# Kernel tuning notes

Measured on AMD Instinct MI355X. Metric: run time of the kernel, lower is better.

## Reference

```python
import jax, jax.numpy as jnp
import numpy as np

D_IN = 768
D_OUT = 768
NUM_HEADS = 12


def setup_inputs() -> dict:
    key = jax.random.key(0)
    kx, kq, kk, kv, ko = jax.random.split(key, 5)
    x = jax.random.normal(kx, (4, 2048, D_IN), dtype=jnp.float32)
    # torch.rand -> uniform [0,1)
    w_query = jax.random.uniform(kq, (D_IN, D_OUT), dtype=jnp.float32)
    w_key = jax.random.uniform(kk, (D_IN, D_OUT), dtype=jnp.float32)
    w_value = jax.random.uniform(kv, (D_IN, D_OUT), dtype=jnp.float32)
    out_proj = jax.random.uniform(ko, (D_IN, D_OUT), dtype=jnp.float32)
    return {"x": x, "w_query": w_query, "w_key": w_key, "w_value": w_value, "out_proj": out_proj}


def reference(x, w_query, w_key, w_value, out_proj):
    b, n, _ = x.shape
    hd = D_OUT // NUM_HEADS  # head_dim
    q = (x @ w_query).reshape(b, n, NUM_HEADS, hd).transpose(0, 2, 1, 3)  # [b,h,n,hd]
    k = (x @ w_key).reshape(b, n, NUM_HEADS, hd).transpose(0, 2, 1, 3)
    v = (x @ w_value).reshape(b, n, NUM_HEADS, hd).transpose(0, 2, 1, 3)
    scores = jnp.einsum('bhqd,bhkd->bhqk', q, k)
    causal = jnp.triu(jnp.ones((n, n), dtype=bool), k=1)
    scores = jnp.where(causal, -jnp.inf, scores)
    attn = jax.nn.softmax(scores / jnp.sqrt(jnp.float32(hd)), axis=-1)
    # dropout p=0.0 -> identity
    ctx = jnp.einsum('bhqk,bhkd->bhqd', attn, v).transpose(0, 2, 1, 3).reshape(b, n, D_OUT)
    return ctx @ out_proj
```

## Files before the change

### kernel.cpp

```cpp
#include <hip/hip_runtime.h>

typedef __bf16    bf16x8 __attribute__((ext_vector_type(8)));
typedef __bf16    bf16x4 __attribute__((ext_vector_type(4)));
typedef _Float16  f16x8  __attribute__((ext_vector_type(8)));
typedef float     f32x4  __attribute__((ext_vector_type(4)));

#define MFMA16(a,b,c)  __builtin_amdgcn_mfma_f32_16x16x32_bf16((a),(b),(c),0,0,0)
#define MFMAF16(a,b,c) __builtin_amdgcn_mfma_f32_16x16x32_f16((a),(b),(c),0,0,0)

#define AS1(p) (const __attribute__((address_space(1))) void*)(p)
#define AS3(p) (__attribute__((address_space(3))) void*)(p)
#define GLL16(g, l) __builtin_amdgcn_global_load_lds(AS1(g), AS3(l), 16, 0, 0)

__device__ __forceinline__ float fexp2(float x) {
  float r; asm("v_exp_f32 %0, %1" : "=v"(r) : "v"(x)); return r;
}

#define QSCALE 0.18033688011112042f

__global__ __launch_bounds__(256) void k_conv_x(const float* __restrict__ x,
                                                __bf16* __restrict__ xh,
                                                __bf16* __restrict__ xl) {
  int i = blockIdx.x * 256 + threadIdx.x;
  const float4* p = (const float4*)x + (size_t)i * 2;
  float4 a = p[0], b = p[1];
  float v[8] = {a.x, a.y, a.z, a.w, b.x, b.y, b.z, b.w};
  bf16x8 h, l;
#pragma unroll
  for (int j = 0; j < 8; ++j) {
    __bf16 hh = (__bf16)v[j];
    h[j] = hh;
    l[j] = (__bf16)(v[j] - (float)hh);
  }
  *(bf16x8*)(xh + (size_t)i * 8) = h;
  *(bf16x8*)(xl + (size_t)i * 8) = l;
}

__global__ __launch_bounds__(256) void k_conv_w(const float* __restrict__ wq,
                                                const float* __restrict__ wk,
                                                const float* __restrict__ wv,
                                                const float* __restrict__ op,
                                                __bf16* __restrict__ wt_h,
                                                __bf16* __restrict__ wt_l,
                                                __bf16* __restrict__ wot) {
  __shared__ float tile[32][33];
  int bid = blockIdx.x;
  int m = bid / 576, rem = bid % 576;
  int tr = rem / 24, tc = rem % 24;
  const float* src = (m == 0) ? wq : (m == 1) ? wk : (m == 2) ? wv : op;
  int tx = threadIdx.x & 31, ty = threadIdx.x >> 5;
  int r0 = tr * 32, c0 = tc * 32;
#pragma unroll
  for (int j = 0; j < 4; ++j)
    tile[ty + j * 8][tx] = src[(size_t)(r0 + ty + j * 8) * 768 + c0 + tx];
  __syncthreads();
#pragma unroll
  for (int j = 0; j < 4; ++j) {
    float v = tile[tx][ty + j * 8];
    size_t o = (size_t)(c0 + ty + j * 8) * 768 + r0 + tx;
    if (m < 3) {
      size_t oo = (size_t)m * (768 * 768) + o;
      __bf16 h = (__bf16)v;
      wt_h[oo] = h;
      wt_l[oo] = (__bf16)(v - (float)h);
    } else {
      wot[o] = (__bf16)v;
    }
  }
}

__global__ __launch_bounds__(256) void k_qkv_gemm(
    const __bf16* __restrict__ Ah, const __bf16* __restrict__ Al,
    const __bf16* __restrict__ Bh, const __bf16* __restrict__ Bl,
    _Float16* __restrict__ qf_o, _Float16* __restrict__ kf_o,
    __bf16* __restrict__ vT_o) {
  __shared__ __align__(16) __bf16 AsH[2][128 * 32];
  __shared__ __align__(16) __bf16 AsL[2][128 * 32];
  __shared__ __align__(16) __bf16 BsH[2][128 * 32];
  __shared__ __align__(16) __bf16 BsL[2][128 * 32];
  int t = threadIdx.x, lane = t & 63, wid = t >> 6;
  int l15 = lane & 15, lh = lane >> 4;
  int bid = blockIdx.x;
  int mt = bid & 63, nt = bid >> 6;
  int m0 = mt * 128, n0 = nt * 128;
  int wr = wid >> 1, wc = wid & 1;
  bool split = (n0 < 1536);
  f32x4 acc[4][4];
#pragma unroll
  for (int i = 0; i < 4; ++i)
#pragma unroll
    for (int j = 0; j < 4; ++j) acc[i][j] = (f32x4){0.f, 0.f, 0.f, 0.f};

  int row0 = t >> 2;
  int kkA = (((t & 3) ^ ((row0 >> 1) & 3)) << 3);
  char* lAH[2] = {(char*)AsH[0] + wid * 1024, (char*)AsH[1] + wid * 1024};
  char* lAL[2] = {(char*)AsL[0] + wid * 1024, (char*)AsL[1] + wid * 1024};
  char* lBH[2] = {(char*)BsH[0] + wid * 1024, (char*)BsH[1] + wid * 1024};
  char* lBL[2] = {(char*)BsL[0] + wid * 1024, (char*)BsL[1] + wid * 1024};

#define QKV_STAGE(bb, k0s) do {                                              \
    size_t a0 = (size_t)(m0 + row0) * 768 + (k0s) + kkA;                     \
    size_t a1 = a0 + (size_t)64 * 768;                                       \
    size_t b0 = (size_t)(n0 + row0) * 768 + (k0s) + kkA;                     \
    size_t b1 = b0 + (size_t)64 * 768;                                       \
    GLL16(Ah + a0, lAH[bb]); GLL16(Ah + a1, lAH[bb] + 4096);                 \
    GLL16(Bh + b0, lBH[bb]); GLL16(Bh + b1, lBH[bb] + 4096);                 \
    if (split) {                                                             \
      GLL16(Al + a0, lAL[bb]); GLL16(Al + a1, lAL[bb] + 4096);               \
      GLL16(Bl + b0, lBL[bb]); GLL16(Bl + b1, lBL[bb] + 4096);               \
    }                                                                        \
  } while (0)

  QKV_STAGE(0, 0);
  asm volatile("s_waitcnt vmcnt(0)" ::: "memory");
  __syncthreads();

  for (int tt = 0; tt < 24; ++tt) {
    int cur = tt & 1;
    if (tt < 23) QKV_STAGE(cur ^ 1, (tt + 1) * 32);

    bf16x8 af[4], alf[4], bf_[4], blf[4];
#pragma unroll
    for (int i = 0; i < 4; ++i) {
      int rowA = wr * 64 + i * 16 + l15;
      int aoff = rowA * 64 + (((lh ^ (rowA >> 1)) & 3) << 4);
      int rowB = wc * 64 + i * 16 + l15;
      int boff = rowB * 64 + (((lh ^ (rowB >> 1)) & 3) << 4);
      af[i]  = *(const bf16x8*)((char*)AsH[cur] + aoff);
      bf_[i] = *(const bf16x8*)((char*)BsH[cur] + boff);
      if (split) {
        alf[i] = *(const bf16x8*)((char*)AsL[cur] + aoff);
        blf[i] = *(const bf16x8*)((char*)BsL[cur] + boff);
      }
    }
#pragma unroll
    for (int i = 0; i < 4; ++i)
#pragma unroll
      for (int j = 0; j < 4; ++j) {
        acc[i][j] = MFMA16(af[i], bf_[j], acc[i][j]);
        if (split) {
          acc[i][j] = MFMA16(af[i], blf[j], acc[i][j]);
          acc[i][j] = MFMA16(alf[i], bf_[j], acc[i][j]);
        }
      }
    asm volatile("s_waitcnt vmcnt(0)" ::: "memory");
    __syncthreads();
  }
#undef QKV_STAGE

#pragma unroll
  for (int j = 0; j < 4; ++j) {
    int c = n0 + wc * 64 + j * 16 + l15;
    int which = c / 768; int cc = c - which * 768;
    int hh = cc >> 6, d = cc & 63;
#pragma unroll
    for (int i = 0; i < 4; ++i)
#pragma unroll
      for (int r = 0; r < 4; ++r) {
        int m = m0 + wr * 64 + i * 16 + lh * 4 + r;
        int bb = m >> 11, n = m & 2047;
        float v = acc[i][j][r];
        if (which == 2) {
          vT_o[((size_t)(bb * 12 + hh) * 64 + d) * 2048 + n] = (__bf16)v;
        } else {
          size_t o = ((size_t)(bb * 12 + hh) * 2048 + n) * 64 + d;
          if (which == 0) qf_o[o] = (_Float16)(v * QSCALE);
          else            kf_o[o] = (_Float16)v;
        }
      }
  }
}

__global__ __launch_bounds__(256) void k_attn(
    const _Float16* __restrict__ Qf, const _Float16* __restrict__ Kf,
    const __bf16* __restrict__ Vt, __bf16* __restrict__ ctx) {
  __shared__ __align__(16) _Float16 Ks[2][64 * 64];
  __shared__ __align__(16) __bf16 Vs[2][64 * 64];
  __shared__ __align__(16) __bf16 Pt[4][32 * 64];
  int t = threadIdx.x, lane = t & 63, wid = t >> 6;
  int l15 = lane & 15, lh = lane >> 4;
  int bid = blockIdx.x;
  int bh = bid % 48;
  int qt = 15 - bid / 48;
  int qbase = qt * 128 + wid * 32;
  size_t base = (size_t)bh * (2048 * 64);
  char* ptw = (char*)Pt[wid];

  int skey = t >> 3, sdb = t & 7;
  int ssw = (sdb ^ (skey & 7)) * 8;
  const _Float16* ksrc = Kf + base + (size_t)skey * 64 + ssw;
  const __bf16* vsrc = Vt + base + (size_t)skey * 2048 + ssw;
  char* dK[2] = {(char*)Ks[0] + wid * 1024, (char*)Ks[1] + wid * 1024};
  char* dV[2] = {(char*)Vs[0] + wid * 1024, (char*)Vs[1] + wid * 1024};

#define ATT_STAGE(bb, k0s) do {                                    \
    GLL16(ksrc + (size_t)(k0s) * 64, dK[bb]);                      \
    GLL16(ksrc + (size_t)(k0s) * 64 + 2048, dK[bb] + 4096);        \
    GLL16(vsrc + (k0s), dV[bb]);                                   \
    GLL16(vsrc + (k0s) + 32 * 2048, dV[bb] + 4096);                \
  } while (0)

  f16x8 qf[2][2];
#pragma unroll
  for (int i = 0; i < 2; ++i)
#pragma unroll
    for (int kk = 0; kk < 2; ++kk)
      qf[i][kk] = *(const f16x8*)(Qf + base +
          (size_t)(qbase + i * 16 + l15) * 64 + kk * 32 + lh * 8);

  f32x4 o[2][4];
#pragma unroll
  for (int i = 0; i < 2; ++i)
#pragma unroll
    for (int d = 0; d < 4; ++d) o[i][d] = (f32x4){0.f, 0.f, 0.f, 0.f};
  float mrun[2] = {-1e30f, -1e30f}, lrun[2] = {0.f, 0.f};

  int nIter = 2 * qt + 2;
  ATT_STAGE(0, 0);
  asm volatile("s_waitcnt vmcnt(0)" ::: "memory");
  __syncthreads();

  for (int it = 0; it < nIter; ++it) {
    int cur = it & 1;
    int k0 = it * 64;
    if (it + 1 < nIter) ATT_STAGE(cur ^ 1, k0 + 64);

    if (k0 <= qbase + 31) {
      f32x4 s[4][2];
#pragma unroll
      for (int j = 0; j < 4; ++j)
#pragma unroll
        for (int i = 0; i < 2; ++i) s[j][i] = (f32x4){0.f, 0.f, 0.f, 0.f};
#pragma unroll
      for (int j = 0; j < 4; ++j) {
        int kr = j * 16 + l15;
#pragma unroll
        for (int kk = 0; kk < 2; ++kk) {
          int sw = ((kk * 4 + lh) ^ (kr & 7)) << 4;
          f16x8 kf = *(const f16x8*)((char*)Ks[cur] + kr * 128 + sw);
          s[j][0] = MFMAF16(kf, qf[0][kk], s[j][0]);
          s[j][1] = MFMAF16(kf, qf[1][kk], s[j][1]);
        }
      }

      if (k0 + 63 > qbase) {
#pragma unroll
        for (int j = 0; j < 4; ++j)
#pragma unroll
          for (int i = 0; i < 2; ++i)
#pragma unroll
            for (int r = 0; r < 4; ++r) {
              int key = k0 + j * 16 + lh * 4 + r;
              int qg = qbase + i * 16 + l15;
              if (key > qg) s[j][i][r] = -1e30f;
            }
      }

#pragma unroll
      for (int i = 0; i < 2; ++i) {
        float m01 = fmaxf(fmaxf(s[0][i][0], s[0][i][1]), fmaxf(s[0][i][2], s[0][i][3]));
        float m23 = fmaxf(fmaxf(s[1][i][0], s[1][i][1]), fmaxf(s[1][i][2], s[1][i][3]));
        float m45 = fmaxf(fmaxf(s[2][i][0], s[2][i][1]), fmaxf(s[2][i][2], s[2][i][3]));
        float m67 = fmaxf(fmaxf(s[3][i][0], s[3][i][1]), fmaxf(s[3][i][2], s[3][i][3]));
        float mx = fmaxf(fmaxf(m01, m23), fmaxf(m45, m67));
        mx = fmaxf(mx, __shfl_xor(mx, 16));
        mx = fmaxf(mx, __shfl_xor(mx, 32));
        float mn = fmaxf(mrun[i], mx);
        float alpha = fexp2(mrun[i] - mn);
        mrun[i] = mn;
        float rsum = 0.f;
#pragma unroll
        for (int j = 0; j < 4; ++j)
#pragma unroll
          for (int r = 0; r < 4; ++r) {
            float e = fexp2(s[j][i][r] - mn);
            s[j][i][r] = e;
            rsum += e;
          }
        rsum += __shfl_xor(rsum, 16);
        rsum += __shfl_xor(rsum, 32);
        lrun[i] = lrun[i] * alpha + rsum;
#pragma unroll
        for (int d = 0; d < 4; ++d) o[i][d] *= alpha;
#pragma unroll
        for (int j = 0; j < 4; ++j) {
          bf16x4 pk = { (__bf16)s[j][i][0], (__bf16)s[j][i][1],
                        (__bf16)s[j][i][2], (__bf16)s[j][i][3] };
          int row = 16 * i + l15;
          int boff = (row * 128 + j * 32 + lh * 8) ^ ((l15 & 7) << 4);
          *(bf16x4*)(ptw + boff) = pk;
        }
      }
      asm volatile("" ::: "memory");
      bf16x8 pa[2][2];
#pragma unroll
      for (int i = 0; i < 2; ++i)
#pragma unroll
        for (int kk = 0; kk < 2; ++kk) {
          int row = 16 * i + l15;
          int boff = (row * 128 + kk * 64 + lh * 16) ^ ((l15 & 7) << 4);
          pa[i][kk] = *(const bf16x8*)(ptw + boff);
        }
      asm volatile("" ::: "memory");

#pragma unroll
      for (int dt = 0; dt < 4; ++dt) {
        int dr = dt * 16 + l15;
#pragma unroll
        for (int kk = 0; kk < 2; ++kk) {
          int sw = ((kk * 4 + lh) ^ (dr & 7)) << 4;
          bf16x8 vf = *(const bf16x8*)((char*)Vs[cur] + dr * 128 + sw);
          o[0][dt] = MFMA16(vf, pa[0][kk], o[0][dt]);
          o[1][dt] = MFMA16(vf, pa[1][kk], o[1][dt]);
        }
      }
    }
    asm volatile("s_waitcnt vmcnt(0)" ::: "memory");
    __syncthreads();
  }
#undef ATT_STAGE

  int b = bh / 12, hh = bh - (bh / 12) * 12;
  float inv[2] = {1.f / lrun[0], 1.f / lrun[1]};
#pragma unroll
  for (int i = 0; i < 2; ++i)
#pragma unroll
    for (int dt = 0; dt < 4; ++dt) {
      bf16x4 cw = { (__bf16)(o[i][dt][0] * inv[i]), (__bf16)(o[i][dt][1] * inv[i]),
                    (__bf16)(o[i][dt][2] * inv[i]), (__bf16)(o[i][dt][3] * inv[i]) };
      int row = 16 * i + l15;
      int boff = (row * 128 + dt * 32 + lh * 8) ^ ((l15 & 7) << 4);
      *(bf16x4*)(ptw + boff) = cw;
    }
  asm volatile("" ::: "memory");
  int lr = lane >> 1, hc = lane & 1;
#pragma unroll
  for (int q16 = 0; q16 < 4; ++q16) {
    int boff = (lr * 128 + hc * 64 + q16 * 16) ^ ((lr & 7) << 4);
    bf16x8 vv = *(const bf16x8*)(ptw + boff);
    *(bf16x8*)(ctx + ((size_t)b * 2048 + qbase + lr) * 768 + hh * 64 + hc * 32 + q16 * 8) = vv;
  }
}

__global__ __launch_bounds__(256) void k_out_gemm(const __bf16* __restrict__ A,
                                                  const __bf16* __restrict__ Bt,
                                                  float* __restrict__ C) {
  __shared__ __align__(16) __bf16 As[2][128 * 32];
  __shared__ __align__(16) __bf16 Bs[2][128 * 32];
  int t = threadIdx.x, lane = t & 63, wid = t >> 6;
  int l15 = lane & 15, lh = lane >> 4;
  int bid = blockIdx.x;
  int mt = bid & 63, nt = bid >> 6;
  int m0 = mt * 128, n0 = nt * 128;
  int wr = wid >> 1, wc = wid & 1;
  f32x4 acc[4][4];
#pragma unroll
  for (int i = 0; i < 4; ++i)
#pragma unroll
    for (int j = 0; j < 4; ++j) acc[i][j] = (f32x4){0.f, 0.f, 0.f, 0.f};
  int row0 = t >> 2;
  int kkA = (((t & 3) ^ ((row0 >> 1) & 3)) << 3);
  char* lA[2] = {(char*)As[0] + wid * 1024, (char*)As[1] + wid * 1024};
  char* lB[2] = {(char*)Bs[0] + wid * 1024, (char*)Bs[1] + wid * 1024};

#define OUT_STAGE(bb, k0s) do {                                              \
    size_t a0 = (size_t)(m0 + row0) * 768 + (k0s) + kkA;                     \
    size_t b0 = (size_t)(n0 + row0) * 768 + (k0s) + kkA;                     \
    GLL16(A + a0, lA[bb]);  GLL16(A + a0 + (size_t)64 * 768, lA[bb] + 4096); \
    GLL16(Bt + b0, lB[bb]); GLL16(Bt + b0 + (size_t)64 * 768, lB[bb] + 4096);\
  } while (0)

  OUT_STAGE(0, 0);
  asm volatile("s_waitcnt vmcnt(0)" ::: "memory");
  __syncthreads();

  for (int tt = 0; tt < 24; ++tt) {
    int cur = tt & 1;
    if (tt < 23) OUT_STAGE(cur ^ 1, (tt + 1) * 32);
    bf16x8 af[4], bf_[4];
#pragma unroll
    for (int i = 0; i < 4; ++i) {
      int rowA = wr * 64 + i * 16 + l15;
      int aoff = rowA * 64 + (((lh ^ (rowA >> 1)) & 3) << 4);
      int rowB = wc * 64 + i * 16 + l15;
      int boff = rowB * 64 + (((lh ^ (rowB >> 1)) & 3) << 4);
      af[i]  = *(const bf16x8*)((char*)As[cur] + aoff);
      bf_[i] = *(const bf16x8*)((char*)Bs[cur] + boff);
    }
#pragma unroll
    for (int i = 0; i < 4; ++i)
#pragma unroll
      for (int j = 0; j < 4; ++j) acc[i][j] = MFMA16(af[i], bf_[j], acc[i][j]);
    asm volatile("s_waitcnt vmcnt(0)" ::: "memory");
    __syncthreads();
  }
#undef OUT_STAGE

#pragma unroll
  for (int j = 0; j < 4; ++j) {
    int c = n0 + wc * 64 + j * 16 + l15;
#pragma unroll
    for (int i = 0; i < 4; ++i)
#pragma unroll
      for (int r = 0; r < 4; ++r) {
        int m = m0 + wr * 64 + i * 16 + lh * 4 + r;
        C[(size_t)m * 768 + c] = acc[i][j][r];
      }
  }
}

extern "C" void kernel_launch(void* const* d_in, const int* in_sizes, int n_in,
                              void* d_out, int out_size, void* d_ws, size_t ws_size,
                              hipStream_t stream) {
  const float* x  = (const float*)d_in[0];
  const float* wq = (const float*)d_in[1];
  const float* wk = (const float*)d_in[2];
  const float* wv = (const float*)d_in[3];
  const float* op = (const float*)d_in[4];
  float* out = (float*)d_out;

  char* ws = (char*)d_ws;
  const size_t SZ = (size_t)8192 * 768 * 2;
  __bf16* xh     = (__bf16*)ws;    ws += SZ;
  __bf16* xl     = (__bf16*)ws;    ws += SZ;
  __bf16* wt_h   = (__bf16*)ws;    ws += (size_t)2304 * 768 * 2;
  __bf16* wt_l   = (__bf16*)ws;    ws += (size_t)2304 * 768 * 2;
  __bf16* wot    = (__bf16*)ws;    ws += (size_t)768 * 768 * 2;
  _Float16* qf   = (_Float16*)ws;  ws += SZ;
  _Float16* kf   = (_Float16*)ws;  ws += SZ;
  __bf16* vT     = (__bf16*)ws;    ws += SZ;
  __bf16* ctx    = (__bf16*)ws;    ws += SZ;

  hipLaunchKernelGGL(k_conv_x, dim3(3072), dim3(256), 0, stream, x, xh, xl);
  hipLaunchKernelGGL(k_conv_w, dim3(2304), dim3(256), 0, stream,
                     wq, wk, wv, op, wt_h, wt_l, wot);
  hipLaunchKernelGGL(k_qkv_gemm, dim3(64 * 18), dim3(256), 0, stream,
                     xh, xl, wt_h, wt_l, qf, kf, vT);
  hipLaunchKernelGGL(k_attn, dim3(48 * 16), dim3(256), 0, stream,
                     qf, kf, vT, ctx);
  hipLaunchKernelGGL(k_out_gemm, dim3(64 * 6), dim3(256), 0, stream, ctx, wot, out);
}
```

Measured before the change: 259.9 us.

## Split QKV GEMM into QK and V kernels, switch V/P/ctx path to fp16, add setprio

```diff
diff --git a/kernel.cpp b/kernel.cpp
--- a/kernel.cpp
+++ b/kernel.cpp
@@ -1,8 +1,8 @@
 #include <hip/hip_runtime.h>
 
 typedef __bf16    bf16x8 __attribute__((ext_vector_type(8)));
-typedef __bf16    bf16x4 __attribute__((ext_vector_type(4)));
 typedef _Float16  f16x8  __attribute__((ext_vector_type(8)));
+typedef _Float16  f16x4  __attribute__((ext_vector_type(4)));
 typedef float     f32x4  __attribute__((ext_vector_type(4)));
 
 #define MFMA16(a,b,c)  __builtin_amdgcn_mfma_f32_16x16x32_bf16((a),(b),(c),0,0,0)
@@ -42,7 +42,7 @@
                                                 const float* __restrict__ op,
                                                 __bf16* __restrict__ wt_h,
                                                 __bf16* __restrict__ wt_l,
-                                                __bf16* __restrict__ wot) {
+                                                _Float16* __restrict__ wot) {
   __shared__ float tile[32][33];
   int bid = blockIdx.x;
   int m = bid / 576, rem = bid % 576;
@@ -64,16 +64,15 @@
       wt_h[oo] = h;
       wt_l[oo] = (__bf16)(v - (float)h);
     } else {
-      wot[o] = (__bf16)v;
+      wot[o] = (_Float16)v;
     }
   }
 }
 
-__global__ __launch_bounds__(256) void k_qkv_gemm(
+__global__ __launch_bounds__(256) void k_qk_gemm(
     const __bf16* __restrict__ Ah, const __bf16* __restrict__ Al,
     const __bf16* __restrict__ Bh, const __bf16* __restrict__ Bl,
-    _Float16* __restrict__ qf_o, _Float16* __restrict__ kf_o,
-    __bf16* __restrict__ vT_o) {
+    _Float16* __restrict__ qf_o, _Float16* __restrict__ kf_o) {
   __shared__ __align__(16) __bf16 AsH[2][128 * 32];
   __shared__ __align__(16) __bf16 AsL[2][128 * 32];
   __shared__ __align__(16) __bf16 BsH[2][128 * 32];
@@ -84,7 +83,6 @@
   int mt = bid & 63, nt = bid >> 6;
   int m0 = mt * 128, n0 = nt * 128;
   int wr = wid >> 1, wc = wid & 1;
-  bool split = (n0 < 1536);
   f32x4 acc[4][4];
 #pragma unroll
   for (int i = 0; i < 4; ++i)
@@ -98,26 +96,24 @@
   char* lBH[2] = {(char*)BsH[0] + wid * 1024, (char*)BsH[1] + wid * 1024};
   char* lBL[2] = {(char*)BsL[0] + wid * 1024, (char*)BsL[1] + wid * 1024};
 
-#define QKV_STAGE(bb, k0s) do {                                              \
+#define QK_STAGE(bb, k0s) do {                                               \
     size_t a0 = (size_t)(m0 + row0) * 768 + (k0s) + kkA;                     \
     size_t a1 = a0 + (size_t)64 * 768;                                       \
     size_t b0 = (size_t)(n0 + row0) * 768 + (k0s) + kkA;                     \
     size_t b1 = b0 + (size_t)64 * 768;                                       \
     GLL16(Ah + a0, lAH[bb]); GLL16(Ah + a1, lAH[bb] + 4096);                 \
     GLL16(Bh + b0, lBH[bb]); GLL16(Bh + b1, lBH[bb] + 4096);                 \
-    if (split) {                                                             \
-      GLL16(Al + a0, lAL[bb]); GLL16(Al + a1, lAL[bb] + 4096);               \
-      GLL16(Bl + b0, lBL[bb]); GLL16(Bl + b1, lBL[bb] + 4096);               \
-    }                                                                        \
+    GLL16(Al + a0, lAL[bb]); GLL16(Al + a1, lAL[bb] + 4096);                 \
+    GLL16(Bl + b0, lBL[bb]); GLL16(Bl + b1, lBL[bb] + 4096);                 \
   } while (0)
 
-  QKV_STAGE(0, 0);
+  QK_STAGE(0, 0);
   asm volatile("s_waitcnt vmcnt(0)" ::: "memory");
   __syncthreads();
 
   for (int tt = 0; tt < 24; ++tt) {
     int cur = tt & 1;
-    if (tt < 23) QKV_STAGE(cur ^ 1, (tt + 1) * 32);
+    if (tt < 23) QK_STAGE(cur ^ 1, (tt + 1) * 32);
 
     bf16x8 af[4], alf[4], bf_[4], blf[4];
 #pragma unroll
@@ -127,26 +123,24 @@
       int rowB = wc * 64 + i * 16 + l15;
       int boff = rowB * 64 + (((lh ^ (rowB >> 1)) & 3) << 4);
       af[i]  = *(const bf16x8*)((char*)AsH[cur] + aoff);
+      alf[i] = *(const bf16x8*)((char*)AsL[cur] + aoff);
       bf_[i] = *(const bf16x8*)((char*)BsH[cur] + boff);
-      if (split) {
-        alf[i] = *(const bf16x8*)((char*)AsL[cur] + aoff);
-        blf[i] = *(const bf16x8*)((char*)BsL[cur] + boff);
-      }
+      blf[i] = *(const bf16x8*)((char*)BsL[cur] + boff);
     }
+    __builtin_amdgcn_s_setprio(1);
 #pragma unroll
     for (int i = 0; i < 4; ++i)
 #pragma unroll
       for (int j = 0; j < 4; ++j) {
         acc[i][j] = MFMA16(af[i], bf_[j], acc[i][j]);
-        if (split) {
-          acc[i][j] = MFMA16(af[i], blf[j], acc[i][j]);
-          acc[i][j] = MFMA16(alf[i], bf_[j], acc[i][j]);
-        }
-      }
+        acc[i][j] = MFMA16(af[i], blf[j], acc[i][j]);
+        acc[i][j] = MFMA16(alf[i], bf_[j], acc[i][j]);
+      }
+    __builtin_amdgcn_s_setprio(0);
     asm volatile("s_waitcnt vmcnt(0)" ::: "memory");
     __syncthreads();
   }
-#undef QKV_STAGE
+#undef QK_STAGE
 
 #pragma unroll
   for (int j = 0; j < 4; ++j) {
@@ -160,23 +154,91 @@
         int m = m0 + wr * 64 + i * 16 + lh * 4 + r;
         int bb = m >> 11, n = m & 2047;
         float v = acc[i][j][r];
-        if (which == 2) {
-          vT_o[((size_t)(bb * 12 + hh) * 64 + d) * 2048 + n] = (__bf16)v;
-        } else {
-          size_t o = ((size_t)(bb * 12 + hh) * 2048 + n) * 64 + d;
-          if (which == 0) qf_o[o] = (_Float16)(v * QSCALE);
-          else            kf_o[o] = (_Float16)v;
-        }
+        size_t o = ((size_t)(bb * 12 + hh) * 2048 + n) * 64 + d;
+        if (which == 0) qf_o[o] = (_Float16)(v * QSCALE);
+        else            kf_o[o] = (_Float16)v;
+      }
+  }
+}
+
+__global__ __launch_bounds__(256) void k_v_gemm(
+    const __bf16* __restrict__ A, const __bf16* __restrict__ Bt,
+    _Float16* __restrict__ vT_o) {
+  __shared__ __align__(16) __bf16 As[2][128 * 32];
+  __shared__ __align__(16) __bf16 Bs[2][128 * 32];
+  int t = threadIdx.x, lane = t & 63, wid = t >> 6;
+  int l15 = lane & 15, lh = lane >> 4;
+  int bid = blockIdx.x;
+  int mt = bid & 63, nt = bid >> 6;
+  int m0 = mt * 128, n0 = 1536 + nt * 128;
+  int wr = wid >> 1, wc = wid & 1;
+  f32x4 acc[4][4];
+#pragma unroll
+  for (int i = 0; i < 4; ++i)
+#pragma unroll
+    for (int j = 0; j < 4; ++j) acc[i][j] = (f32x4){0.f, 0.f, 0.f, 0.f};
+  int row0 = t >> 2;
+  int kkA = (((t & 3) ^ ((row0 >> 1) & 3)) << 3);
+  char* lA[2] = {(char*)As[0] + wid * 1024, (char*)As[1] + wid * 1024};
+  char* lB[2] = {(char*)Bs[0] + wid * 1024, (char*)Bs[1] + wid * 1024};
+
+#define V_STAGE(bb, k0s) do {                                                \
+    size_t a0 = (size_t)(m0 + row0) * 768 + (k0s) + kkA;                     \
+    size_t b0 = (size_t)(n0 + row0) * 768 + (k0s) + kkA;                     \
+    GLL16(A + a0, lA[bb]);  GLL16(A + a0 + (size_t)64 * 768, lA[bb] + 4096); \
+    GLL16(Bt + b0, lB[bb]); GLL16(Bt + b0 + (size_t)64 * 768, lB[bb] + 4096);\
+  } while (0)
+
+  V_STAGE(0, 0);
+  asm volatile("s_waitcnt vmcnt(0)" ::: "memory");
+  __syncthreads();
+
+  for (int tt = 0; tt < 24; ++tt) {
+    int cur = tt & 1;
+    if (tt < 23) V_STAGE(cur ^ 1, (tt + 1) * 32);
+    bf16x8 af[4], bf_[4];
+#pragma unroll
+    for (int i = 0; i < 4; ++i) {
+      int rowA = wr * 64 + i * 16 + l15;
+      int aoff = rowA * 64 + (((lh ^ (rowA >> 1)) & 3) << 4);
+      int rowB = wc * 64 + i * 16 + l15;
+      int boff = rowB * 64 + (((lh ^ (rowB >> 1)) & 3) << 4);
+      af[i]  = *(const bf16x8*)((char*)As[cur] + aoff);
+      bf_[i] = *(const bf16x8*)((char*)Bs[cur] + boff);
+    }
+    __builtin_amdgcn_s_setprio(1);
+#pragma unroll
+    for (int i = 0; i < 4; ++i)
+#pragma unroll
+      for (int j = 0; j < 4; ++j) acc[i][j] = MFMA16(af[i], bf_[j], acc[i][j]);
+    __builtin_amdgcn_s_setprio(0);
+    asm volatile("s_waitcnt vmcnt(0)" ::: "memory");
+    __syncthreads();
+  }
+#undef V_STAGE
+
+#pragma unroll
+  for (int j = 0; j < 4; ++j) {
+    int c = n0 + wc * 64 + j * 16 + l15;
+    int cc = c - 1536;
+    int hh = cc >> 6, d = cc & 63;
+#pragma unroll
+    for (int i = 0; i < 4; ++i)
+#pragma unroll
+      for (int r = 0; r < 4; ++r) {
+        int m = m0 + wr * 64 + i * 16 + lh * 4 + r;
+        int bb = m >> 11, n = m & 2047;
+        vT_o[((size_t)(bb * 12 + hh) * 64 + d) * 2048 + n] = (_Float16)acc[i][j][r];
       }
   }
 }
 
 __global__ __launch_bounds__(256) void k_attn(
     const _Float16* __restrict__ Qf, const _Float16* __restrict__ Kf,
-    const __bf16* __restrict__ Vt, __bf16* __restrict__ ctx) {
+    const _Float16* __restrict__ Vt, _Float16* __restrict__ ctx) {
   __shared__ __align__(16) _Float16 Ks[2][64 * 64];
-  __shared__ __align__(16) __bf16 Vs[2][64 * 64];
-  __shared__ __align__(16) __bf16 Pt[4][32 * 64];
+  __shared__ __align__(16) _Float16 Vs[2][64 * 64];
+  __shared__ __align__(16) _Float16 Pt[4][32 * 64];
   int t = threadIdx.x, lane = t & 63, wid = t >> 6;
   int l15 = lane & 15, lh = lane >> 4;
   int bid = blockIdx.x;
@@ -189,7 +251,7 @@
   int skey = t >> 3, sdb = t & 7;
   int ssw = (sdb ^ (skey & 7)) * 8;
   const _Float16* ksrc = Kf + base + (size_t)skey * 64 + ssw;
-  const __bf16* vsrc = Vt + base + (size_t)skey * 2048 + ssw;
+  const _Float16* vsrc = Vt + base + (size_t)skey * 2048 + ssw;
   char* dK[2] = {(char*)Ks[0] + wid * 1024, (char*)Ks[1] + wid * 1024};
   char* dV[2] = {(char*)Vs[0] + wid * 1024, (char*)Vs[1] + wid * 1024};
 
@@ -231,6 +293,7 @@
       for (int j = 0; j < 4; ++j)
 #pragma unroll
         for (int i = 0; i < 2; ++i) s[j][i] = (f32x4){0.f, 0.f, 0.f, 0.f};
+      __builtin_amdgcn_s_setprio(1);
 #pragma unroll
       for (int j = 0; j < 4; ++j) {
         int kr = j * 16 + l15;
@@ -242,6 +305,7 @@
           s[j][1] = MFMAF16(kf, qf[1][kk], s[j][1]);
         }
       }
+      __builtin_amdgcn_s_setprio(0);
 
       if (k0 + 63 > qbase) {
 #pragma unroll
@@ -284,36 +348,38 @@
         for (int d = 0; d < 4; ++d) o[i][d] *= alpha;
 #pragma unroll
         for (int j = 0; j < 4; ++j) {
-          bf16x4 pk = { (__bf16)s[j][i][0], (__bf16)s[j][i][1],
-                        (__bf16)s[j][i][2], (__bf16)s[j][i][3] };
+          f16x4 pk = { (_Float16)s[j][i][0], (_Float16)s[j][i][1],
+                       (_Float16)s[j][i][2], (_Float16)s[j][i][3] };
           int row = 16 * i + l15;
           int boff = (row * 128 + j * 32 + lh * 8) ^ ((l15 & 7) << 4);
-          *(bf16x4*)(ptw + boff) = pk;
+          *(f16x4*)(ptw + boff) = pk;
         }
       }
       asm volatile("" ::: "memory");
-      bf16x8 pa[2][2];
+      f16x8 pa[2][2];
 #pragma unroll
       for (int i = 0; i < 2; ++i)
 #pragma unroll
         for (int kk = 0; kk < 2; ++kk) {
           int row = 16 * i + l15;
           int boff = (row * 128 + kk * 64 + lh * 16) ^ ((l15 & 7) << 4);
-          pa[i][kk] = *(const bf16x8*)(ptw + boff);
+          pa[i][kk] = *(const f16x8*)(ptw + boff);
         }
       asm volatile("" ::: "memory");
 
+      __builtin_amdgcn_s_setprio(1);
 #pragma unroll
       for (int dt = 0; dt < 4; ++dt) {
         int dr = dt * 16 + l15;
 #pragma unroll
         for (int kk = 0; kk < 2; ++kk) {
           int sw = ((kk * 4 + lh) ^ (dr & 7)) << 4;
-          bf16x8 vf = *(const bf16x8*)((char*)Vs[cur] + dr * 128 + sw);
-          o[0][dt] = MFMA16(vf, pa[0][kk], o[0][dt]);
-          o[1][dt] = MFMA16(vf, pa[1][kk], o[1][dt]);
+          f16x8 vf = *(const f16x8*)((char*)Vs[cur] + dr * 128 + sw);
+          o[0][dt] = MFMAF16(vf, pa[0][kk], o[0][dt]);
+          o[1][dt] = MFMAF16(vf, pa[1][kk], o[1][dt]);
         }
       }
+      __builtin_amdgcn_s_setprio(0);
     }
     asm volatile("s_waitcnt vmcnt(0)" ::: "memory");
     __syncthreads();
@@ -326,27 +392,27 @@
   for (int i = 0; i < 2; ++i)
 #pragma unroll
     for (int dt = 0; dt < 4; ++dt) {
-      bf16x4 cw = { (__bf16)(o[i][dt][0] * inv[i]), (__bf16)(o[i][dt][1] * inv[i]),
-                    (__bf16)(o[i][dt][2] * inv[i]), (__bf16)(o[i][dt][3] * inv[i]) };
+      f16x4 cw = { (_Float16)(o[i][dt][0] * inv[i]), (_Float16)(o[i][dt][1] * inv[i]),
+                   (_Float16)(o[i][dt][2] * inv[i]), (_Float16)(o[i][dt][3] * inv[i]) };
       int row = 16 * i + l15;
       int boff = (row * 128 + dt * 32 + lh * 8) ^ ((l15 & 7) << 4);
-      *(bf16x4*)(ptw + boff) = cw;
+      *(f16x4*)(ptw + boff) = cw;
     }
   asm volatile("" ::: "memory");
   int lr = lane >> 1, hc = lane & 1;
 #pragma unroll
   for (int q16 = 0; q16 < 4; ++q16) {
     int boff = (lr * 128 + hc * 64 + q16 * 16) ^ ((lr & 7) << 4);
-    bf16x8 vv = *(const bf16x8*)(ptw + boff);
-    *(bf16x8*)(ctx + ((size_t)b * 2048 + qbase + lr) * 768 + hh * 64 + hc * 32 + q16 * 8) = vv;
-  }
-}
-
-__global__ __launch_bounds__(256) void k_out_gemm(const __bf16* __restrict__ A,
-                                                  const __bf16* __restrict__ Bt,
+    f16x8 vv = *(const f16x8*)(ptw + boff);
+    *(f16x8*)(ctx + ((size_t)b * 2048 + qbase + lr) * 768 + hh * 64 + hc * 32 + q16 * 8) = vv;
+  }
+}
+
+__global__ __launch_bounds__(256) void k_out_gemm(const _Float16* __restrict__ A,
+                                                  const _Float16* __restrict__ Bt,
                                                   float* __restrict__ C) {
-  __shared__ __align__(16) __bf16 As[2][128 * 32];
-  __shared__ __align__(16) __bf16 Bs[2][128 * 32];
+  __shared__ __align__(16) _Float16 As[2][128 * 32];
+  __shared__ __align__(16) _Float16 Bs[2][128 * 32];
   int t = threadIdx.x, lane = t & 63, wid = t >> 6;
   int l15 = lane & 15, lh = lane >> 4;
   int bid = blockIdx.x;
@@ -377,20 +443,22 @@
   for (int tt = 0; tt < 24; ++tt) {
     int cur = tt & 1;
     if (tt < 23) OUT_STAGE(cur ^ 1, (tt + 1) * 32);
-    bf16x8 af[4], bf_[4];
+    f16x8 af[4], bf_[4];
 #pragma unroll
     for (int i = 0; i < 4; ++i) {
       int rowA = wr * 64 + i * 16 + l15;
       int aoff = rowA * 64 + (((lh ^ (rowA >> 1)) & 3) << 4);
       int rowB = wc * 64 + i * 16 + l15;
       int boff = rowB * 64 + (((lh ^ (rowB >> 1)) & 3) << 4);
-      af[i]  = *(const bf16x8*)((char*)As[cur] + aoff);
-      bf_[i] = *(const bf16x8*)((char*)Bs[cur] + boff);
+      af[i]  = *(const f16x8*)((char*)As[cur] + aoff);
+      bf_[i] = *(const f16x8*)((char*)Bs[cur] + boff);
     }
+    __builtin_amdgcn_s_setprio(1);
 #pragma unroll
     for (int i = 0; i < 4; ++i)
 #pragma unroll
-      for (int j = 0; j < 4; ++j) acc[i][j] = MFMA16(af[i], bf_[j], acc[i][j]);
+      for (int j = 0; j < 4; ++j) acc[i][j] = MFMAF16(af[i], bf_[j], acc[i][j]);
+    __builtin_amdgcn_s_setprio(0);
     asm volatile("s_waitcnt vmcnt(0)" ::: "memory");
     __syncthreads();
   }
@@ -425,18 +493,18 @@
   __bf16* xl     = (__bf16*)ws;    ws += SZ;
   __bf16* wt_h   = (__bf16*)ws;    ws += (size_t)2304 * 768 * 2;
   __bf16* wt_l   = (__bf16*)ws;    ws += (size_t)2304 * 768 * 2;
-  __bf16* wot    = (__bf16*)ws;    ws += (size_t)768 * 768 * 2;
+  _Float16* wot  = (_Float16*)ws;  ws += (size_t)768 * 768 * 2;
   _Float16* qf   = (_Float16*)ws;  ws += SZ;
   _Float16* kf   = (_Float16*)ws;  ws += SZ;
-  __bf16* vT     = (__bf16*)ws;    ws += SZ;
-  __bf16* ctx    = (__bf16*)ws;    ws += SZ;
+  _Float16* vT   = (_Float16*)ws;  ws += SZ;
+  _Float16* ctx  = (_Float16*)ws;  ws += SZ;
 
   hipLaunchKernelGGL(k_conv_x, dim3(3072), dim3(256), 0, stream, x, xh, xl);
   hipLaunchKernelGGL(k_conv_w, dim3(2304), dim3(256), 0, stream,
                      wq, wk, wv, op, wt_h, wt_l, wot);
-  hipLaunchKernelGGL(k_qkv_gemm, dim3(64 * 18), dim3(256), 0, stream,
-                     xh, xl, wt_h, wt_l, qf, kf, vT);
-  hipLaunchKernelGGL(k_attn, dim3(48 * 16), dim3(256), 0, stream,
-                     qf, kf, vT, ctx);
+  hipLaunchKernelGGL(k_qk_gemm, dim3(64 * 12), dim3(256), 0, stream,
+                     xh, xl, wt_h, wt_l, qf, kf);
+  hipLaunchKernelGGL(k_v_gemm, dim3(64 * 6), dim3(256), 0, stream, xh, wt_h, vT);
+  hipLaunchKernelGGL(k_attn, dim3(48 * 16), dim3(256), 0, stream, qf, kf, vT, ctx);
   hipLaunchKernelGGL(k_out_gemm, dim3(64 * 6), dim3(256), 0, stream, ctx, wot, out);
 }
```

Measured after the change: 246.6 us. 5.1% less time.
